# Kernel optimization log

Measured on AMD Instinct MI355X. Metric: run time of the kernel, lower is better.

## Reference

```python
import jax, jax.numpy as jnp
from jax import lax
import numpy as np

BS, C_IN, C_OUT, STYLE_D, H, W, F = 8, 256, 256, 512, 64, 64, 3


def setup_inputs() -> dict:
    key = jax.random.key(0)
    k = jax.random.split(key, 6)
    # xavier_uniform for conv weight: gain=1, fan_in=c_in*f*f, fan_out=c_out*f*f
    fan_in, fan_out = C_IN * F * F, C_OUT * F * F
    limit_w = float(np.sqrt(6.0 / (fan_in + fan_out)))
    limit_a = float(np.sqrt(1.0 / STYLE_D))  # torch Linear default init bound
    return {
        "x": jax.random.normal(k[0], (BS, C_IN, H, W), jnp.float32),
        "s": jax.random.normal(k[1], (BS, STYLE_D), jnp.float32),
        "w": jax.random.uniform(k[2], (C_OUT, C_IN, F, F), jnp.float32, -limit_w, limit_w),
        "b": jnp.zeros((C_OUT, 1, 1), jnp.float32),
        "affine_w": jax.random.uniform(k[3], (C_IN, STYLE_D), jnp.float32, -limit_a, limit_a),
        "affine_b": jax.random.uniform(k[4], (C_IN,), jnp.float32, -limit_a, limit_a),
    }


def reference(x, s, w, b, affine_w, affine_b):
    bs = x.shape[0]
    # style -> per-channel modulation scales: [bs, c_in]
    style = s @ affine_w.T + affine_b
    # modulate: [bs, c_out, c_in, f, f]
    wmod = w[None, :, :, :, :] * (style[:, None, :, None, None] + 1.0)
    # demodulate
    d = jnp.sqrt(jnp.sum(jnp.square(wmod), axis=(2, 3, 4), keepdims=True) + 1e-8)
    wmod = wmod / d
    # grouped conv with groups=bs (per-sample weights)
    xr = x.reshape(1, bs * x.shape[1], x.shape[2], x.shape[3])
    cw = wmod.reshape(bs * wmod.shape[1], wmod.shape[2], wmod.shape[3], wmod.shape[4])
    out = lax.conv_general_dilated(
        xr, cw, window_strides=(1, 1), padding=((1, 1), (1, 1)),
        dimension_numbers=("NCHW", "OIHW", "NCHW"), feature_group_count=bs)
    out = out.reshape(bs, wmod.shape[1], out.shape[2], out.shape[3])
    return out + b  # b broadcasts as [c_out,1,1]
```

## Files before the change

### kernel.cpp

```cpp
#include <hip/hip_runtime.h>
#include <hip/hip_bf16.h>
#include <stdint.h>

#define BS   8
#define CIN  256
#define COUT 256
#define SD   512
#define HH   64
#define WW   64
#define HP   66

typedef __attribute__((ext_vector_type(8))) short short8;
typedef __attribute__((ext_vector_type(4))) float f32x4;

__device__ __forceinline__ unsigned short f2bf(float f) {
    __hip_bfloat16 h = __float2bfloat16(f);
    return *reinterpret_cast<unsigned short*>(&h);
}

typedef __attribute__((address_space(3))) unsigned int lds_u32_t;
typedef const __attribute__((address_space(1))) unsigned int glb_u32_t;

__device__ __forceinline__ void async16(const void* g, void* l) {
    __builtin_amdgcn_global_load_lds((glb_u32_t*)g, (lds_u32_t*)l, 16, 0, 0);
}

#define VMCNT(n) asm volatile("s_waitcnt vmcnt(" #n ")" ::: "memory")
#define SCHED_FENCE() __builtin_amdgcn_sched_barrier(0)

__global__ void k_style(const float* __restrict__ s, const float* __restrict__ aw,
                        const float* __restrict__ ab, float* __restrict__ m) {
    int b = blockIdx.x >> 3, chunk = blockIdx.x & 7;
    int tid = threadIdx.x;
    __shared__ float sv[SD];
    for (int d = tid; d < SD; d += 256) sv[d] = s[b * SD + d];
    __syncthreads();
    int il = tid >> 3, p = tid & 7;
    int i = chunk * 32 + il;
    const float4* awr = (const float4*)(aw + (size_t)i * SD + p * 64);
    float acc = 0.f;
#pragma unroll
    for (int d4 = 0; d4 < 16; ++d4) {
        float4 w4 = awr[d4];
        int d0 = p * 64 + d4 * 4;
        acc += w4.x * sv[d0] + w4.y * sv[d0 + 1] + w4.z * sv[d0 + 2] + w4.w * sv[d0 + 3];
    }
    acc += __shfl_xor(acc, 1);
    acc += __shfl_xor(acc, 2);
    acc += __shfl_xor(acc, 4);
    if (p == 0) m[b * CIN + i] = acc + ab[i] + 1.0f;
}

__global__ void k_prep(const float* __restrict__ w, const float* __restrict__ m,
                       const float* __restrict__ x,
                       unsigned short* __restrict__ wb, float* __restrict__ dinv,
                       unsigned short* __restrict__ xp) {
    __shared__ float red[4][8];
    int tid = threadIdx.x;

    if (blockIdx.x < COUT) {
        int o = blockIdx.x, i = tid;
        const float* wp = w + ((size_t)o * CIN + i) * 9;
        float v[9];
        float q = 0.f;
#pragma unroll
        for (int t = 0; t < 9; ++t) { v[t] = wp[t]; q += v[t] * v[t]; }
#pragma unroll
        for (int t = 0; t < 9; ++t)
            wb[((size_t)t * COUT + o) * CIN + i] = f2bf(v[t]);

        float r[8];
#pragma unroll
        for (int b = 0; b < 8; ++b) {
            float mv = m[b * CIN + i];
            r[b] = q * mv * mv;
        }
#pragma unroll
        for (int b = 0; b < 8; ++b) {
            r[b] += __shfl_xor(r[b], 1);
            r[b] += __shfl_xor(r[b], 2);
            r[b] += __shfl_xor(r[b], 4);
            r[b] += __shfl_xor(r[b], 8);
            r[b] += __shfl_xor(r[b], 16);
            r[b] += __shfl_xor(r[b], 32);
        }
        int lane = i & 63, wid = i >> 6;
        if (lane == 0) {
#pragma unroll
            for (int b = 0; b < 8; ++b) red[wid][b] = r[b];
        }
        __syncthreads();
        if (i < 8) {
            float acc = red[0][i] + red[1][i] + red[2][i] + red[3][i];
            dinv[i * COUT + o] = rsqrtf(acc + 1e-8f);
        }
        return;
    }

    int bi = blockIdx.x - COUT;
    int b = bi / HP, yp = bi % HP;
    unsigned short* row = xp + ((size_t)(b * HP + yp)) * HP * CIN;

    if (yp == 0 || yp == HP - 1) {
        uint4 z = {0u, 0u, 0u, 0u};
        uint4* r = (uint4*)row;
        for (int j = tid; j < HP * CIN / 8; j += 256) r[j] = z;
        return;
    }
    int y = yp - 1;

    if (tid < 64) {
        uint4 z = {0u, 0u, 0u, 0u};
        if (tid < 32) ((uint4*)row)[tid] = z;
        else ((uint4*)(row + (size_t)(HP - 1) * CIN))[tid - 32] = z;
    }

#pragma unroll
    for (int it = 0; it < 2; ++it) {
        int u = it * 256 + tid;
        int x0 = (u & 15) * 4;
        int i0 = (u >> 4) * 8;
        float vv[8][4];
        float mv[8];
#pragma unroll
        for (int k = 0; k < 8; ++k) {
            *(float4*)vv[k] = *(const float4*)&x[(((size_t)b * CIN + i0 + k) * HH + y) * WW + x0];
            mv[k] = m[b * CIN + i0 + k];
        }
#pragma unroll
        for (int j = 0; j < 4; ++j) {
            short8 p;
#pragma unroll
            for (int k = 0; k < 8; ++k)
                p[k] = (short)f2bf(vv[k][j] * mv[k]);
            *(short8*)&row[(size_t)(x0 + j + 1) * CIN + i0] = p;
        }
    }
}

__global__ void __launch_bounds__(256, 2)
k_conv(const unsigned short* __restrict__ xp,
       const unsigned short* __restrict__ wb,
       const float* __restrict__ dinv,
       const float* __restrict__ bias,
       float* __restrict__ out) {
    __shared__ unsigned short Ar[3168 * 8];
    __shared__ unsigned short Bs[3 * 512 * 8];

    int bx = blockIdx.x;
    int mt = bx & 127;
    int n0 = (bx >> 7) << 6;
    int m0 = mt << 8;
    int b  = m0 >> 12;
    int y0 = (m0 >> 6) & 63;

    int tid = threadIdx.x;
    int lane = tid & 63, w = tid >> 6;
    int quad = lane >> 4, mrow = lane & 15;

    f32x4 acc[4][4] = {};

    const unsigned short* xb = xp + (size_t)b * HP * HP * CIN;

    auto stageA = [&](int kc) {
        int ch0 = kc * 64;
#pragma unroll
        for (int k = 0; k < 12; ++k) {
            int sA = k * 256 + tid;
            int rowA = sA / 528;
            int rem = sA - rowA * 528;
            int colA = rem >> 3, c4 = rem & 7;
            async16(xb + ((size_t)(y0 + rowA) * HP + colA) * CIN + ch0 + ((c4 ^ (colA & 7)) << 3),
                    &Ar[sA * 8]);
        }
        if (tid < 96) {
            int sA = 3072 + tid;
            int rowA = sA / 528;
            int rem = sA - rowA * 528;
            int colA = rem >> 3, c4 = rem & 7;
            async16(xb + ((size_t)(y0 + rowA) * HP + colA) * CIN + ch0 + ((c4 ^ (colA & 7)) << 3),
                    &Ar[sA * 8]);
        }
    };

    auto stageB = [&](int tt, int kcc, int buf) {
        const unsigned short* bp = wb + ((size_t)tt * COUT + n0) * CIN + kcc * 64;
        unsigned short* dst = Bs + buf * 4096;
#pragma unroll
        for (int k = 0; k < 2; ++k) {
            int sB = k * 256 + tid;
            int rowB = sB >> 3, c4 = sB & 7;
            async16(bp + (size_t)rowB * CIN + ((c4 ^ (rowB & 7)) << 3), dst + sB * 8);
        }
    };

    stageA(0);
    stageB(0, 0, 0);
    stageB(1, 0, 1);
    VMCNT(2);
    __builtin_amdgcn_s_barrier();
    SCHED_FENCE();

#pragma unroll 1
    for (int kc = 0; kc < 4; ++kc) {
#pragma unroll
        for (int t = 0; t < 9; ++t) {
            if (t < 7) stageB(t + 2, kc, (t + 2) % 3);
            else if (kc < 3) stageB(t - 7, kc + 1, (t + 2) % 3);

            int dy = t / 3, dx = t - dy * 3;
            int arow = w + dy;
            const unsigned short* Bcur = Bs + (t % 3) * 4096;

            short8 af[2][4], bf[2][4];
#pragma unroll
            for (int h = 0; h < 2; ++h)
#pragma unroll
                for (int i = 0; i < 4; ++i) {
                    int col = mrow + i * 16 + dx;
                    int chunk = arow * 528 + col * 8 + ((h * 4 + quad) ^ (col & 7));
                    af[h][i] = *(const short8*)&Ar[chunk * 8];
                }
#pragma unroll
            for (int h = 0; h < 2; ++h)
#pragma unroll
                for (int j = 0; j < 4; ++j) {
                    int rowB = mrow + j * 16;
                    int chunk = rowB * 8 + ((h * 4 + quad) ^ (rowB & 7));
                    bf[h][j] = *(const short8*)&Bcur[chunk * 8];
                }
#pragma unroll
            for (int h = 0; h < 2; ++h)
#pragma unroll
                for (int i = 0; i < 4; ++i)
#pragma unroll
                    for (int j = 0; j < 4; ++j)
                        acc[i][j] = __builtin_amdgcn_mfma_f32_16x16x32_bf16(
                            af[h][i], bf[h][j], acc[i][j], 0, 0, 0);

            if (t < 8) {
                if (kc == 3 && t == 7) {
                    VMCNT(0);
                } else {
                    VMCNT(2);
                }
                __builtin_amdgcn_s_barrier();
                SCHED_FENCE();
            } else if (kc < 3) {
                VMCNT(2);
                __builtin_amdgcn_s_barrier();
                SCHED_FENCE();
                stageA(kc + 1);
                VMCNT(0);
                __builtin_amdgcn_s_barrier();
                SCHED_FENCE();
            }
        }
    }

    int y = y0 + w;
#pragma unroll
    for (int j = 0; j < 4; ++j) {
        int o = n0 + mrow + j * 16;
        float dv = dinv[b * COUT + o];
        float bv = bias[o];
#pragma unroll
        for (int i = 0; i < 4; ++i) {
            int xx = i * 16 + quad * 4;
            f32x4 v = acc[i][j] * dv + bv;
            *(f32x4*)(out + (((size_t)(b * COUT + o) * HH + y) * WW + xx)) = v;
        }
    }
}

extern "C" void kernel_launch(void* const* d_in, const int* in_sizes, int n_in,
                              void* d_out, int out_size, void* d_ws, size_t ws_size,
                              hipStream_t stream) {
    const float* x    = (const float*)d_in[0];
    const float* s    = (const float*)d_in[1];
    const float* w    = (const float*)d_in[2];
    const float* bias = (const float*)d_in[3];
    const float* aw   = (const float*)d_in[4];
    const float* ab   = (const float*)d_in[5];
    float* out = (float*)d_out;

    char* ws = (char*)d_ws;
    float* m            = (float*)(ws + 0);
    float* dinv         = (float*)(ws + 8192);
    unsigned short* wb  = (unsigned short*)(ws + 16384);
    unsigned short* xpb = (unsigned short*)(ws + 1196032);

    k_style<<<64, 256, 0, stream>>>(s, aw, ab, m);
    k_prep<<<COUT + BS * HP, 256, 0, stream>>>(w, m, x, wb, dinv, xpb);
    k_conv<<<512, 256, 0, stream>>>(xpb, wb, dinv, bias, out);
}
```

Before: 136.0 us.

## Load conv weight fragments directly from global into registers, dropping LDS B staging

Removes the triple-buffered LDS staging of weight tiles. Each thread now loads its MFMA B fragments straight from global memory into registers, ping-ponging between two register sets so the next tap's weights are prefetched during the current tap's MFMAs. This drops the per-tap barriers and LDS writes and reads for B, and frees LDS. The cost is more register pressure and uncoalesced 16-byte global loads that all four waves duplicate, served from L2.

```diff
diff --git a/kernel.cpp b/kernel.cpp
--- a/kernel.cpp
+++ b/kernel.cpp
@@ -145,7 +145,6 @@
        const float* __restrict__ bias,
        float* __restrict__ out) {
     __shared__ unsigned short Ar[3168 * 8];
-    __shared__ unsigned short Bs[3 * 512 * 8];
 
     int bx = blockIdx.x;
     int mt = bx & 127;
@@ -161,6 +160,7 @@
     f32x4 acc[4][4] = {};
 
     const unsigned short* xb = xp + (size_t)b * HP * HP * CIN;
+    const unsigned short* wbase = wb + ((size_t)(n0 + mrow)) * CIN + quad * 8;
 
     auto stageA = [&](int kc) {
         int ch0 = kc * 64;
@@ -183,80 +183,84 @@
         }
     };
 
-    auto stageB = [&](int tt, int kcc, int buf) {
-        const unsigned short* bp = wb + ((size_t)tt * COUT + n0) * CIN + kcc * 64;
-        unsigned short* dst = Bs + buf * 4096;
-#pragma unroll
-        for (int k = 0; k < 2; ++k) {
-            int sB = k * 256 + tid;
-            int rowB = sB >> 3, c4 = sB & 7;
-            async16(bp + (size_t)rowB * CIN + ((c4 ^ (rowB & 7)) << 3), dst + sB * 8);
-        }
-    };
+#define LDB(T, KC, H, J) \
+    (*(const short8*)(wbase + ((size_t)(T) * COUT + (J) * 16) * CIN + (KC) * 64 + (H) * 32))
+
+#define LOADB(S, T, KC) do { \
+    S##0 = LDB(T, KC, 0, 0); S##1 = LDB(T, KC, 0, 1); \
+    S##2 = LDB(T, KC, 0, 2); S##3 = LDB(T, KC, 0, 3); \
+    S##4 = LDB(T, KC, 1, 0); S##5 = LDB(T, KC, 1, 1); \
+    S##6 = LDB(T, KC, 1, 2); S##7 = LDB(T, KC, 1, 3); } while (0)
+
+#define RDA(DY, DX, H, I) \
+    (*(const short8*)&Ar[(size_t)((w + (DY)) * 528 + (mrow + (I) * 16 + (DX)) * 8 + \
+        (((H) * 4 + quad) ^ ((mrow + (I) * 16 + (DX)) & 7))) * 8])
+
+#define LOADA(T) do { \
+    A0 = RDA((T) / 3, (T) % 3, 0, 0); A1 = RDA((T) / 3, (T) % 3, 0, 1); \
+    A2 = RDA((T) / 3, (T) % 3, 0, 2); A3 = RDA((T) / 3, (T) % 3, 0, 3); \
+    A4 = RDA((T) / 3, (T) % 3, 1, 0); A5 = RDA((T) / 3, (T) % 3, 1, 1); \
+    A6 = RDA((T) / 3, (T) % 3, 1, 2); A7 = RDA((T) / 3, (T) % 3, 1, 3); } while (0)
+
+#define MFMA1(a, bb, c) __builtin_amdgcn_mfma_f32_16x16x32_bf16(a, bb, c, 0, 0, 0)
+
+#define TAPMFMA(S) do { \
+    acc[0][0] = MFMA1(A0, S##0, acc[0][0]); acc[0][1] = MFMA1(A0, S##1, acc[0][1]); \
+    acc[0][2] = MFMA1(A0, S##2, acc[0][2]); acc[0][3] = MFMA1(A0, S##3, acc[0][3]); \
+    acc[1][0] = MFMA1(A1, S##0, acc[1][0]); acc[1][1] = MFMA1(A1, S##1, acc[1][1]); \
+    acc[1][2] = MFMA1(A1, S##2, acc[1][2]); acc[1][3] = MFMA1(A1, S##3, acc[1][3]); \
+    acc[2][0] = MFMA1(A2, S##0, acc[2][0]); acc[2][1] = MFMA1(A2, S##1, acc[2][1]); \
+    acc[2][2] = MFMA1(A2, S##2, acc[2][2]); acc[2][3] = MFMA1(A2, S##3, acc[2][3]); \
+    acc[3][0] = MFMA1(A3, S##0, acc[3][0]); acc[3][1] = MFMA1(A3, S##1, acc[3][1]); \
+    acc[3][2] = MFMA1(A3, S##2, acc[3][2]); acc[3][3] = MFMA1(A3, S##3, acc[3][3]); \
+    acc[0][0] = MFMA1(A4, S##4, acc[0][0]); acc[0][1] = MFMA1(A4, S##5, acc[0][1]); \
+    acc[0][2] = MFMA1(A4, S##6, acc[0][2]); acc[0][3] = MFMA1(A4, S##7, acc[0][3]); \
+    acc[1][0] = MFMA1(A5, S##4, acc[1][0]); acc[1][1] = MFMA1(A5, S##5, acc[1][1]); \
+    acc[1][2] = MFMA1(A5, S##6, acc[1][2]); acc[1][3] = MFMA1(A5, S##7, acc[1][3]); \
+    acc[2][0] = MFMA1(A6, S##4, acc[2][0]); acc[2][1] = MFMA1(A6, S##5, acc[2][1]); \
+    acc[2][2] = MFMA1(A6, S##6, acc[2][2]); acc[2][3] = MFMA1(A6, S##7, acc[2][3]); \
+    acc[3][0] = MFMA1(A7, S##4, acc[3][0]); acc[3][1] = MFMA1(A7, S##5, acc[3][1]); \
+    acc[3][2] = MFMA1(A7, S##6, acc[3][2]); acc[3][3] = MFMA1(A7, S##7, acc[3][3]); } while (0)
+
+#define TAP(T, CS, NS) do { \
+    if ((T) < 8) LOADB(NS, (T) + 1, kc); \
+    LOADA(T); \
+    TAPMFMA(CS); } while (0)
+
+    short8 P0, P1, P2, P3, P4, P5, P6, P7;
+    short8 Q0, Q1, Q2, Q3, Q4, Q5, Q6, Q7;
+    short8 A0, A1, A2, A3, A4, A5, A6, A7;
 
     stageA(0);
-    stageB(0, 0, 0);
-    stageB(1, 0, 1);
-    VMCNT(2);
+    LOADB(P, 0, 0);
+    VMCNT(0);
     __builtin_amdgcn_s_barrier();
     SCHED_FENCE();
 
 #pragma unroll 1
     for (int kc = 0; kc < 4; ++kc) {
-#pragma unroll
-        for (int t = 0; t < 9; ++t) {
-            if (t < 7) stageB(t + 2, kc, (t + 2) % 3);
-            else if (kc < 3) stageB(t - 7, kc + 1, (t + 2) % 3);
-
-            int dy = t / 3, dx = t - dy * 3;
-            int arow = w + dy;
-            const unsigned short* Bcur = Bs + (t % 3) * 4096;
-
-            short8 af[2][4], bf[2][4];
-#pragma unroll
-            for (int h = 0; h < 2; ++h)
-#pragma unroll
-                for (int i = 0; i < 4; ++i) {
-                    int col = mrow + i * 16 + dx;
-                    int chunk = arow * 528 + col * 8 + ((h * 4 + quad) ^ (col & 7));
-                    af[h][i] = *(const short8*)&Ar[chunk * 8];
-                }
-#pragma unroll
-            for (int h = 0; h < 2; ++h)
-#pragma unroll
-                for (int j = 0; j < 4; ++j) {
-                    int rowB = mrow + j * 16;
-                    int chunk = rowB * 8 + ((h * 4 + quad) ^ (rowB & 7));
-                    bf[h][j] = *(const short8*)&Bcur[chunk * 8];
-                }
-#pragma unroll
-            for (int h = 0; h < 2; ++h)
-#pragma unroll
-                for (int i = 0; i < 4; ++i)
-#pragma unroll
-                    for (int j = 0; j < 4; ++j)
-                        acc[i][j] = __builtin_amdgcn_mfma_f32_16x16x32_bf16(
-                            af[h][i], bf[h][j], acc[i][j], 0, 0, 0);
-
-            if (t < 8) {
-                if (kc == 3 && t == 7) {
-                    VMCNT(0);
-                } else {
-                    VMCNT(2);
-                }
-                __builtin_amdgcn_s_barrier();
-                SCHED_FENCE();
-            } else if (kc < 3) {
-                VMCNT(2);
-                __builtin_amdgcn_s_barrier();
-                SCHED_FENCE();
-                stageA(kc + 1);
-                VMCNT(0);
-                __builtin_amdgcn_s_barrier();
-                SCHED_FENCE();
-            }
-        }
-    }
+        TAP(0, P, Q); TAP(1, Q, P); TAP(2, P, Q);
+        TAP(3, Q, P); TAP(4, P, Q); TAP(5, Q, P);
+        TAP(6, P, Q); TAP(7, Q, P); TAP(8, P, Q);
+
+        if (kc < 3) {
+            __builtin_amdgcn_s_barrier();
+            SCHED_FENCE();
+            stageA(kc + 1);
+            LOADB(P, 0, kc + 1);
+            VMCNT(0);
+            __builtin_amdgcn_s_barrier();
+            SCHED_FENCE();
+        }
+    }
+
+#undef TAP
+#undef TAPMFMA
+#undef MFMA1
+#undef LOADA
+#undef RDA
+#undef LOADB
+#undef LDB
 
     int y = y0 + w;
 #pragma unroll
```

Result: slower. 171.9 us (+26.5%).
